# Optimization experiments

Hardware: AMD Instinct MI355X
Metric: run time of the kernel (lower is better)

## Reference

```python
import jax, jax.numpy as jnp
import numpy as np
import math

MAX_REL_POS = 32  # max_relative_position

def _sincos_table(d_model, max_len):
    pos = np.arange(max_len)[:, None].astype(np.float32)
    div = np.exp(np.arange(0, d_model, 2).astype(np.float32) * (-math.log(10000.0) / d_model))
    pe = np.zeros((max_len, d_model), dtype=np.float32)
    pe[:, 0::2] = np.sin(pos * div)
    pe[:, 1::2] = np.cos(pos * div)
    return jnp.asarray(pe)

def setup_inputs() -> dict:
    rng = jax.random.key(0)
    k1, k2, k3 = jax.random.split(rng, 3)
    B, H, S, D = 4, 16, 1024, 64
    pe = _sincos_table(D, 2 * MAX_REL_POS + 1)  # fixed (non-trainable) buffer
    return {
        "query": jax.random.normal(k1, (B, H, S, D), jnp.float32),
        "key": jax.random.normal(k2, (B, H, S, D), jnp.float32),
        "value": jax.random.normal(k3, (B, H, S, D), jnp.float32),
        "pe_k": pe,
        "pe_v": pe,
    }

def reference(query, key, value, pe_k, pe_v):
    B, H, S, D = query.shape
    # relative distance indices: clip(k - q, -P, P) + P  -> [S, S]
    dist = jnp.clip(jnp.arange(S)[None, :] - jnp.arange(S)[:, None],
                    -MAX_REL_POS, MAX_REL_POS) + MAX_REL_POS
    R_k = pe_k[dist]  # [S, S, D]
    R_v = pe_v[dist]  # [S, S, D]
    scores = jnp.einsum('bhqd,bhkd->bhqk', query, key)
    scores = scores + jnp.einsum('bhqd,qkd->bhqk', query, R_k)
    scores = scores / math.sqrt(D)
    # one_direction=True -> causal mask
    causal = jnp.tril(jnp.ones((S, S), dtype=bool))
    scores = jnp.where(causal[None, None], scores, jnp.float32(-1e9))
    p_attn = jax.nn.softmax(scores, axis=-1)
    output = jnp.einsum('bhqk,bhkd->bhqd', p_attn, value)
    output = output + jnp.einsum('bhqv,qvd->bhqd', p_attn, R_v)
    return output, p_attn
```

## Files before the change

### kernel.cpp

```cpp
#include <hip/hip_runtime.h>
#include <math.h>

typedef __attribute__((ext_vector_type(8))) short bfrag;
typedef __attribute__((ext_vector_type(4))) float ffrag;

namespace {
constexpr int Sc = 1024, Dc = 64;
constexpr int P2 = 72;
constexpr int PQ = 64;
constexpr int PW = 33;
constexpr float S2 = 0.125f * 1.44269504088896f;
}

__device__ __forceinline__ unsigned short f2bf(float f) {
    unsigned u = __builtin_bit_cast(unsigned, f);
    u += 0x7fffu + ((u >> 16) & 1u);
    return (unsigned short)(u >> 16);
}
__device__ __forceinline__ bfrag pack8(float4 a, float4 b) {
    bfrag r;
    r[0] = (short)f2bf(a.x); r[1] = (short)f2bf(a.y);
    r[2] = (short)f2bf(a.z); r[3] = (short)f2bf(a.w);
    r[4] = (short)f2bf(b.x); r[5] = (short)f2bf(b.y);
    r[6] = (short)f2bf(b.z); r[7] = (short)f2bf(b.w);
    return r;
}
#define MFMA(a, b, c) __builtin_amdgcn_mfma_f32_16x16x32_bf16((a), (b), (c), 0, 0, 0)

__global__ __launch_bounds__(256, 2)
void relattn(const float* __restrict__ Qg, const float* __restrict__ Kg,
             const float* __restrict__ Vg, const float* __restrict__ pek,
             const float* __restrict__ pev, float* __restrict__ outg,
             float* __restrict__ pbuf)
{
    __shared__ __align__(16) char smem[72448];
    unsigned short* Ks0 = (unsigned short*)smem;
    unsigned short* Ks1 = (unsigned short*)(smem + 9216);
    unsigned short* Vt0 = (unsigned short*)(smem + 18432);
    unsigned short* Vt1 = (unsigned short*)(smem + 27648);
    unsigned short* Pt0 = (unsigned short*)(smem + 36864);
    unsigned short* Pt1 = (unsigned short*)(smem + 46080);
    float* Ts = (float*)(smem + 55296);
    unsigned short* Qs = (unsigned short*)(smem + 63744);
    float* Ws = (float*)(smem + 63744);
    float* W0 = (float*)(smem + 72192);
    float* Ot = (float*)smem;

    const int tid  = threadIdx.x;
    const int bh   = blockIdx.y;
    const int wv   = tid >> 6;
    const int lane = tid & 63;
    const int n    = lane & 15;
    const int quad = lane >> 4;

    const float* Qbh = Qg + (size_t)bh * Sc * Dc;
    const float* Kbh = Kg + (size_t)bh * Sc * Dc;
    const float* Vbh = Vg + (size_t)bh * Sc * Dc;
    float* pbh = pbuf + (size_t)bh * Sc * Sc;
    float* obh = outg + (size_t)bh * Sc * Dc;

    const int sr  = tid >> 2;
    const int sc4 = (tid & 3) * 16;
    const int kp  = tid & 31;
    const int vd0 = (tid >> 5) * 8;

    const int rr = tid >> 4;
    const int c4 = tid & 15;

    for (int half = 0; half < 2; ++half) {
        const int qt = half ? (15 - (int)blockIdx.x) : (int)blockIdx.x;
        const int qrow = wv * 16 + quad * 4;

        __syncthreads();

        {
            const float* src = Qbh + (size_t)(qt * 64 + sr) * Dc + sc4;
            float4 a = *(const float4*)(src);
            float4 b = *(const float4*)(src + 4);
            float4 c = *(const float4*)(src + 8);
            float4 d = *(const float4*)(src + 12);
            *(bfrag*)&Qs[sr * PQ + sc4]     = pack8(a, b);
            *(bfrag*)&Qs[sr * PQ + sc4 + 8] = pack8(c, d);
        }
        for (int i = tid; i < 135; i += 256) {
            bfrag z = {};
            *(bfrag*)&Ks0[33 * P2 + i * 8] = z;
        }
        if (tid < 132) {
            int r = tid >> 2, c0 = (tid & 3) * 16;
            const float* src = pek + (size_t)r * Dc + c0;
            float4 a = *(const float4*)(src);
            float4 b = *(const float4*)(src + 4);
            float4 c = *(const float4*)(src + 8);
            float4 d = *(const float4*)(src + 12);
            *(bfrag*)&Ks0[r * P2 + c0]     = pack8(a, b);
            *(bfrag*)&Ks0[r * P2 + c0 + 8] = pack8(c, d);
        }
        __syncthreads();

        bfrag qa0 = *(bfrag*)&Qs[(wv * 16 + n) * PQ + quad * 8];
        bfrag qa1 = *(bfrag*)&Qs[(wv * 16 + n) * PQ + 32 + quad * 8];

        #pragma unroll
        for (int sub = 0; sub < 3; ++sub) {
            bfrag b0 = *(bfrag*)&Ks0[(sub * 16 + n) * P2 + quad * 8];
            bfrag b1 = *(bfrag*)&Ks0[(sub * 16 + n) * P2 + 32 + quad * 8];
            ffrag c = {};
            c = MFMA(qa0, b0, c);
            c = MFMA(qa1, b1, c);
            int j = sub * 16 + n;
            if (j <= 32) {
                #pragma unroll
                for (int reg = 0; reg < 4; ++reg)
                    Ts[(qrow + reg) * PW + j] = c[reg];
            }
        }
        __syncthreads();

        float ts2[4];
        #pragma unroll
        for (int reg = 0; reg < 4; ++reg) ts2[reg] = Ts[(qrow + reg) * PW] * S2;

        for (int idx = tid; idx < 64 * PW; idx += 256) Ws[idx] = 0.f;

        {
            const int zb = (qt + 1) * 64;
            if (zb < Sc) {
                const int z4 = (Sc - zb) >> 2;
                const float4 z = make_float4(0.f, 0.f, 0.f, 0.f);
                for (int r = 0; r < 64; ++r) {
                    float4* rp = (float4*)(pbh + (size_t)(qt * 64 + r) * Sc + zb);
                    for (int cz = tid; cz < z4; cz += 256) rp[cz] = z;
                }
            }
        }

        float lsum[4] = {0.f, 0.f, 0.f, 0.f};
        {
            const float* kfp = Kbh + (size_t)n * Dc + quad * 8;
            for (int kt = 0; kt <= qt; ++kt) {
                const bool bnd = (kt >= qt - 1);
                const float* kpt = kfp + (size_t)(kt * 64) * Dc;
                float4 r0[4], r1[4], r2[4], r3[4];
                #pragma unroll
                for (int s = 0; s < 4; ++s) {
                    const float* ps = kpt + (size_t)(s * 16) * Dc;
                    r0[s] = *(const float4*)(ps);
                    r1[s] = *(const float4*)(ps + 4);
                    r2[s] = *(const float4*)(ps + 32);
                    r3[s] = *(const float4*)(ps + 36);
                }
                #pragma unroll
                for (int s = 0; s < 4; ++s) {
                    bfrag b0 = pack8(r0[s], r1[s]);
                    bfrag b1 = pack8(r2[s], r3[s]);
                    ffrag c = {};
                    c = MFMA(qa0, b0, c);
                    c = MFMA(qa1, b1, c);
                    const int k = kt * 64 + s * 16 + n;
                    if (!bnd) {
                        #pragma unroll
                        for (int reg = 0; reg < 4; ++reg)
                            lsum[reg] += exp2f(fmaf(c[reg], S2, ts2[reg]));
                    } else {
                        #pragma unroll
                        for (int reg = 0; reg < 4; ++reg) {
                            int jrel = k - (qt * 64 + qrow + reg) + 32;
                            if (jrel <= 32) {
                                int jcl = jrel < 0 ? 0 : jrel;
                                lsum[reg] += exp2f(fmaf(c[reg] + Ts[(qrow + reg) * PW + jcl], S2, 0.f));
                            }
                        }
                    }
                }
            }
        }
        float rinv[4];
        #pragma unroll
        for (int reg = 0; reg < 4; ++reg) {
            float l = lsum[reg];
            l += __shfl_xor(l, 1);
            l += __shfl_xor(l, 2);
            l += __shfl_xor(l, 4);
            l += __shfl_xor(l, 8);
            rinv[reg] = 1.f / l;
        }

        {
            const float* ksrc = Kbh + (size_t)sr * Dc + sc4;
            float4 a = *(const float4*)(ksrc);
            float4 b = *(const float4*)(ksrc + 4);
            float4 c = *(const float4*)(ksrc + 8);
            float4 d = *(const float4*)(ksrc + 12);
            *(bfrag*)&Ks0[sr * P2 + sc4]     = pack8(a, b);
            *(bfrag*)&Ks0[sr * P2 + sc4 + 8] = pack8(c, d);
        }
        float4 pka, pkb, pkc, pkd;
        if (qt >= 1) {
            const float* ksrc = Kbh + (size_t)(64 + sr) * Dc + sc4;
            pka = *(const float4*)(ksrc);
            pkb = *(const float4*)(ksrc + 4);
            pkc = *(const float4*)(ksrc + 8);
            pkd = *(const float4*)(ksrc + 12);
        }
        float4 pva, pvb, pvc, pvd;
        {
            const float* vsrc = Vbh + (size_t)(2 * kp) * Dc + vd0;
            pva = *(const float4*)(vsrc);
            pvb = *(const float4*)(vsrc + 4);
            pvc = *(const float4*)(vsrc + Dc);
            pvd = *(const float4*)(vsrc + Dc + 4);
        }
        __syncthreads();

        ffrag oacc[4];
        #pragma unroll
        for (int i = 0; i < 4; ++i) { ffrag z = {}; oacc[i] = z; }

        for (int kt = 0; kt <= qt; ++kt) {
            const bool bnd = (kt >= qt - 1);
            unsigned short* Kc  = (kt & 1) ? Ks1 : Ks0;
            unsigned short* Kn  = (kt & 1) ? Ks0 : Ks1;
            unsigned short* Vc  = (kt & 1) ? Vt1 : Vt0;
            unsigned short* Vp  = (kt & 1) ? Vt0 : Vt1;
            unsigned short* Ptc = (kt & 1) ? Pt1 : Pt0;
            unsigned short* Ptp = (kt & 1) ? Pt0 : Pt1;

            #pragma unroll
            for (int sub = 0; sub < 4; ++sub) {
                bfrag b0 = *(bfrag*)&Kc[(sub * 16 + n) * P2 + quad * 8];
                bfrag b1 = *(bfrag*)&Kc[(sub * 16 + n) * P2 + 32 + quad * 8];
                ffrag c = {};
                c = MFMA(qa0, b0, c);
                c = MFMA(qa1, b1, c);
                const int k = kt * 64 + sub * 16 + n;
                if (!bnd) {
                    #pragma unroll
                    for (int reg = 0; reg < 4; ++reg) {
                        float p = exp2f(fmaf(c[reg], S2, ts2[reg])) * rinv[reg];
                        Ptc[(qrow + reg) * P2 + sub * 16 + n] = (unsigned short)f2bf(p);
                    }
                } else {
                    #pragma unroll
                    for (int reg = 0; reg < 4; ++reg) {
                        int jrel = k - (qt * 64 + qrow + reg) + 32;
                        float p = 0.f;
                        if (jrel <= 32) {
                            int jcl = jrel < 0 ? 0 : jrel;
                            p = exp2f((c[reg] + Ts[(qrow + reg) * PW + jcl]) * S2) * rinv[reg];
                        }
                        Ptc[(qrow + reg) * P2 + sub * 16 + n] = (unsigned short)f2bf(p);
                        if ((unsigned)(jrel - 1) < 32u) Ws[(qrow + reg) * PW + jrel - 1] = p;
                    }
                }
            }
            if (kt < qt) {
                *(bfrag*)&Kn[sr * P2 + sc4]     = pack8(pka, pkb);
                *(bfrag*)&Kn[sr * P2 + sc4 + 8] = pack8(pkc, pkd);
            }
            {
                float r0[8] = {pva.x, pva.y, pva.z, pva.w, pvb.x, pvb.y, pvb.z, pvb.w};
                float r1[8] = {pvc.x, pvc.y, pvc.z, pvc.w, pvd.x, pvd.y, pvd.z, pvd.w};
                #pragma unroll
                for (int i = 0; i < 8; ++i) {
                    unsigned pk2 = (unsigned)f2bf(r0[i]) | ((unsigned)f2bf(r1[i]) << 16);
                    *(unsigned*)&Vc[(vd0 + i) * P2 + 2 * kp] = pk2;
                }
            }
            if (kt + 2 <= qt) {
                const float* ksrc = Kbh + (size_t)((kt + 2) * 64 + sr) * Dc + sc4;
                pka = *(const float4*)(ksrc);
                pkb = *(const float4*)(ksrc + 4);
                pkc = *(const float4*)(ksrc + 8);
                pkd = *(const float4*)(ksrc + 12);
            }
            if (kt + 1 <= qt) {
                const float* vsrc = Vbh + (size_t)((kt + 1) * 64 + 2 * kp) * Dc + vd0;
                pva = *(const float4*)(vsrc);
                pvb = *(const float4*)(vsrc + 4);
                pvc = *(const float4*)(vsrc + Dc);
                pvd = *(const float4*)(vsrc + Dc + 4);
            }
            if (kt >= 1) {
                bfrag pb0 = *(bfrag*)&Ptp[(wv * 16 + n) * P2 + quad * 8];
                bfrag pb1 = *(bfrag*)&Ptp[(wv * 16 + n) * P2 + 32 + quad * 8];
                #pragma unroll
                for (int ds = 0; ds < 4; ++ds) {
                    bfrag va0 = *(bfrag*)&Vp[(ds * 16 + n) * P2 + quad * 8];
                    bfrag va1 = *(bfrag*)&Vp[(ds * 16 + n) * P2 + 32 + quad * 8];
                    oacc[ds] = MFMA(va0, pb0, oacc[ds]);
                    oacc[ds] = MFMA(va1, pb1, oacc[ds]);
                }
                float* base = pbh + ((size_t)(qt * 64 + rr) * Sc + (kt - 1) * 64 + c4 * 4);
                #pragma unroll
                for (int step = 0; step < 4; ++step) {
                    const int r = step * 16 + rr;
                    uint2 two = *(const uint2*)&Ptp[r * P2 + c4 * 4];
                    float4 v;
                    v.x = __builtin_bit_cast(float, (two.x & 0xffffu) << 16);
                    v.y = __builtin_bit_cast(float, two.x & 0xffff0000u);
                    v.z = __builtin_bit_cast(float, (two.y & 0xffffu) << 16);
                    v.w = __builtin_bit_cast(float, two.y & 0xffff0000u);
                    *(float4*)(base + (size_t)(step * 16) * Sc) = v;
                }
            }
            __syncthreads();
        }
        {
            unsigned short* Ptp = (qt & 1) ? Pt1 : Pt0;
            unsigned short* Vp  = (qt & 1) ? Vt1 : Vt0;
            bfrag pb0 = *(bfrag*)&Ptp[(wv * 16 + n) * P2 + quad * 8];
            bfrag pb1 = *(bfrag*)&Ptp[(wv * 16 + n) * P2 + 32 + quad * 8];
            #pragma unroll
            for (int ds = 0; ds < 4; ++ds) {
                bfrag va0 = *(bfrag*)&Vp[(ds * 16 + n) * P2 + quad * 8];
                bfrag va1 = *(bfrag*)&Vp[(ds * 16 + n) * P2 + 32 + quad * 8];
                oacc[ds] = MFMA(va0, pb0, oacc[ds]);
                oacc[ds] = MFMA(va1, pb1, oacc[ds]);
            }
            float* base = pbh + ((size_t)(qt * 64 + rr) * Sc + qt * 64 + c4 * 4);
            #pragma unroll
            for (int step = 0; step < 4; ++step) {
                const int r = step * 16 + rr;
                uint2 two = *(const uint2*)&Ptp[r * P2 + c4 * 4];
                float4 v;
                v.x = __builtin_bit_cast(float, (two.x & 0xffffu) << 16);
                v.y = __builtin_bit_cast(float, two.x & 0xffff0000u);
                v.z = __builtin_bit_cast(float, (two.y & 0xffffu) << 16);
                v.w = __builtin_bit_cast(float, two.y & 0xffff0000u);
                *(float4*)(base + (size_t)(step * 16) * Sc) = v;
            }
        }
        __syncthreads();

        if (tid < 64) {
            float s = 0.f;
            #pragma unroll
            for (int j = 0; j < 32; ++j) s += Ws[tid * PW + j];
            W0[tid] = 1.f - s;
        }
        {
            int q = tid >> 2, j0 = (tid & 3) * 8;
            #pragma unroll
            for (int i = 0; i < 8; i += 2) {
                unsigned pk2 = (unsigned)f2bf(Ws[q * PW + j0 + i]) |
                               ((unsigned)f2bf(Ws[q * PW + j0 + i + 1]) << 16);
                *(unsigned*)&Pt0[q * P2 + j0 + i] = pk2;
            }
        }
        {
            int jj = tid >> 3, d0 = (tid & 7) * 8;
            const float* src = pev + (size_t)(jj + 1) * Dc + d0;
            float4 a = *(const float4*)(src);
            float4 b = *(const float4*)(src + 4);
            float vr[8] = {a.x, a.y, a.z, a.w, b.x, b.y, b.z, b.w};
            #pragma unroll
            for (int i = 0; i < 8; ++i)
                Vt0[(d0 + i) * P2 + jj] = (unsigned short)f2bf(vr[i]);
        }
        __syncthreads();
        {
            bfrag pb = *(bfrag*)&Pt0[(wv * 16 + n) * P2 + quad * 8];
            #pragma unroll
            for (int ds = 0; ds < 4; ++ds) {
                bfrag va = *(bfrag*)&Vt0[(ds * 16 + n) * P2 + quad * 8];
                oacc[ds] = MFMA(va, pb, oacc[ds]);
            }
        }
        float w0q = W0[wv * 16 + n];
        #pragma unroll
        for (int ds = 0; ds < 4; ++ds) {
            float4 ov;
            ov.x = oacc[ds][0] + w0q * pev[ds * 16 + quad * 4 + 0];
            ov.y = oacc[ds][1] + w0q * pev[ds * 16 + quad * 4 + 1];
            ov.z = oacc[ds][2] + w0q * pev[ds * 16 + quad * 4 + 2];
            ov.w = oacc[ds][3] + w0q * pev[ds * 16 + quad * 4 + 3];
            *(float4*)&Ot[(wv * 16 + n) * 68 + ds * 16 + quad * 4] = ov;
        }
        __syncthreads();
        {
            int r = tid >> 2, c0 = (tid & 3) * 16;
            float* dst = obh + (size_t)(qt * 64 + r) * Dc + c0;
            *(float4*)(dst)      = *(float4*)&Ot[r * 68 + c0];
            *(float4*)(dst + 4)  = *(float4*)&Ot[r * 68 + c0 + 4];
            *(float4*)(dst + 8)  = *(float4*)&Ot[r * 68 + c0 + 8];
            *(float4*)(dst + 12) = *(float4*)&Ot[r * 68 + c0 + 12];
        }
    }
}

extern "C" void kernel_launch(void* const* d_in, const int* in_sizes, int n_in,
                              void* d_out, int out_size, void* d_ws, size_t ws_size,
                              hipStream_t stream)
{
    const float* Q   = (const float*)d_in[0];
    const float* K   = (const float*)d_in[1];
    const float* V   = (const float*)d_in[2];
    const float* pek = (const float*)d_in[3];
    const float* pev = (const float*)d_in[4];
    float* out  = (float*)d_out;
    float* pbuf = out + (size_t)64 * Sc * Dc;

    dim3 grid(8, 64);
    relattn<<<grid, 256, 0, stream>>>(Q, K, V, pek, pev, out, pbuf);
}
```

Before: 411.4 us.

## Stage K tiles through shared memory in the row-sum pass

The first pass, which computes the softmax row sums, used to have each wave load its own K fragments straight from global memory and convert them per wave. It now loads each K tile cooperatively into shared memory as bf16, in groups of three tiles. The groups are double-buffered across the Ks, Vt and Pt buffers, with register prefetch of the next group. This removes redundant global loads across the four waves, at the cost of extra shared-memory traffic, a barrier per group, and more registers held for prefetch.

```diff
diff --git a/kernel.cpp b/kernel.cpp
--- a/kernel.cpp
+++ b/kernel.cpp
@@ -73,6 +73,17 @@
 
         __syncthreads();
 
+        float4 pka[3], pkb[3], pkc[3], pkd[3];
+        #pragma unroll
+        for (int t = 0; t < 3; ++t) {
+            if (t <= qt) {
+                const float* ksrc = Kbh + (size_t)(t * 64 + sr) * Dc + sc4;
+                pka[t] = *(const float4*)(ksrc);
+                pkb[t] = *(const float4*)(ksrc + 4);
+                pkc[t] = *(const float4*)(ksrc + 8);
+                pkd[t] = *(const float4*)(ksrc + 12);
+            }
+        }
         {
             const float* src = Qbh + (size_t)(qt * 64 + sr) * Dc + sc4;
             float4 a = *(const float4*)(src);
@@ -84,7 +95,7 @@
         }
         for (int i = tid; i < 135; i += 256) {
             bfrag z = {};
-            *(bfrag*)&Ks0[33 * P2 + i * 8] = z;
+            *(bfrag*)&Pt1[33 * P2 + i * 8] = z;
         }
         if (tid < 132) {
             int r = tid >> 2, c0 = (tid & 3) * 16;
@@ -93,8 +104,8 @@
             float4 b = *(const float4*)(src + 4);
             float4 c = *(const float4*)(src + 8);
             float4 d = *(const float4*)(src + 12);
-            *(bfrag*)&Ks0[r * P2 + c0]     = pack8(a, b);
-            *(bfrag*)&Ks0[r * P2 + c0 + 8] = pack8(c, d);
+            *(bfrag*)&Pt1[r * P2 + c0]     = pack8(a, b);
+            *(bfrag*)&Pt1[r * P2 + c0 + 8] = pack8(c, d);
         }
         __syncthreads();
 
@@ -103,8 +114,8 @@
 
         #pragma unroll
         for (int sub = 0; sub < 3; ++sub) {
-            bfrag b0 = *(bfrag*)&Ks0[(sub * 16 + n) * P2 + quad * 8];
-            bfrag b1 = *(bfrag*)&Ks0[(sub * 16 + n) * P2 + 32 + quad * 8];
+            bfrag b0 = *(bfrag*)&Pt1[(sub * 16 + n) * P2 + quad * 8];
+            bfrag b1 = *(bfrag*)&Pt1[(sub * 16 + n) * P2 + 32 + quad * 8];
             ffrag c = {};
             c = MFMA(qa0, b0, c);
             c = MFMA(qa1, b1, c);
@@ -115,6 +126,24 @@
                     Ts[(qrow + reg) * PW + j] = c[reg];
             }
         }
+        #pragma unroll
+        for (int t = 0; t < 3; ++t) {
+            if (t <= qt) {
+                unsigned short* Bn = t == 0 ? Ks0 : (t == 1 ? Ks1 : Vt0);
+                *(bfrag*)&Bn[sr * P2 + sc4]     = pack8(pka[t], pkb[t]);
+                *(bfrag*)&Bn[sr * P2 + sc4 + 8] = pack8(pkc[t], pkd[t]);
+            }
+        }
+        #pragma unroll
+        for (int t = 0; t < 3; ++t) {
+            if (3 + t <= qt) {
+                const float* ksrc = Kbh + (size_t)((3 + t) * 64 + sr) * Dc + sc4;
+                pka[t] = *(const float4*)(ksrc);
+                pkb[t] = *(const float4*)(ksrc + 4);
+                pkc[t] = *(const float4*)(ksrc + 8);
+                pkd[t] = *(const float4*)(ksrc + 12);
+            }
+        }
         __syncthreads();
 
         float ts2[4];
@@ -136,44 +165,64 @@
         }
 
         float lsum[4] = {0.f, 0.f, 0.f, 0.f};
-        {
-            const float* kfp = Kbh + (size_t)n * Dc + quad * 8;
-            for (int kt = 0; kt <= qt; ++kt) {
-                const bool bnd = (kt >= qt - 1);
-                const float* kpt = kfp + (size_t)(kt * 64) * Dc;
-                float4 r0[4], r1[4], r2[4], r3[4];
-                #pragma unroll
-                for (int s = 0; s < 4; ++s) {
-                    const float* ps = kpt + (size_t)(s * 16) * Dc;
-                    r0[s] = *(const float4*)(ps);
-                    r1[s] = *(const float4*)(ps + 4);
-                    r2[s] = *(const float4*)(ps + 32);
-                    r3[s] = *(const float4*)(ps + 36);
-                }
-                #pragma unroll
-                for (int s = 0; s < 4; ++s) {
-                    bfrag b0 = pack8(r0[s], r1[s]);
-                    bfrag b1 = pack8(r2[s], r3[s]);
-                    ffrag c = {};
-                    c = MFMA(qa0, b0, c);
-                    c = MFMA(qa1, b1, c);
-                    const int k = kt * 64 + s * 16 + n;
-                    if (!bnd) {
-                        #pragma unroll
-                        for (int reg = 0; reg < 4; ++reg)
-                            lsum[reg] += exp2f(fmaf(c[reg], S2, ts2[reg]));
-                    } else {
-                        #pragma unroll
-                        for (int reg = 0; reg < 4; ++reg) {
-                            int jrel = k - (qt * 64 + qrow + reg) + 32;
-                            if (jrel <= 32) {
-                                int jcl = jrel < 0 ? 0 : jrel;
-                                lsum[reg] += exp2f(fmaf(c[reg] + Ts[(qrow + reg) * PW + jcl], S2, 0.f));
+        for (int kt = 0; kt <= qt; kt += 3) {
+            const int ph = (kt / 3) & 1;
+            unsigned short* Bc0 = ph ? Vt1 : Ks0;
+            unsigned short* Bc1 = ph ? Pt0 : Ks1;
+            unsigned short* Bc2 = ph ? Pt1 : Vt0;
+            unsigned short* Bn0 = ph ? Ks0 : Vt1;
+            unsigned short* Bn1 = ph ? Ks1 : Pt0;
+            unsigned short* Bn2 = ph ? Vt0 : Pt1;
+
+            #pragma unroll
+            for (int t = 0; t < 3; ++t) {
+                if (kt + t <= qt) {
+                    unsigned short* Bc = t == 0 ? Bc0 : (t == 1 ? Bc1 : Bc2);
+                    const bool bnd = (kt + t >= qt - 1);
+                    #pragma unroll
+                    for (int sub = 0; sub < 4; ++sub) {
+                        bfrag b0 = *(bfrag*)&Bc[(sub * 16 + n) * P2 + quad * 8];
+                        bfrag b1 = *(bfrag*)&Bc[(sub * 16 + n) * P2 + 32 + quad * 8];
+                        ffrag c = {};
+                        c = MFMA(qa0, b0, c);
+                        c = MFMA(qa1, b1, c);
+                        const int k = (kt + t) * 64 + sub * 16 + n;
+                        if (!bnd) {
+                            #pragma unroll
+                            for (int reg = 0; reg < 4; ++reg)
+                                lsum[reg] += exp2f(fmaf(c[reg], S2, ts2[reg]));
+                        } else {
+                            #pragma unroll
+                            for (int reg = 0; reg < 4; ++reg) {
+                                int jrel = k - (qt * 64 + qrow + reg) + 32;
+                                if (jrel <= 32) {
+                                    int jcl = jrel < 0 ? 0 : jrel;
+                                    lsum[reg] += exp2f(fmaf(c[reg] + Ts[(qrow + reg) * PW + jcl], S2, 0.f));
+                                }
                             }
                         }
                     }
                 }
             }
+            #pragma unroll
+            for (int t = 0; t < 3; ++t) {
+                if (kt + 3 + t <= qt) {
+                    unsigned short* Bn = t == 0 ? Bn0 : (t == 1 ? Bn1 : Bn2);
+                    *(bfrag*)&Bn[sr * P2 + sc4]     = pack8(pka[t], pkb[t]);
+                    *(bfrag*)&Bn[sr * P2 + sc4 + 8] = pack8(pkc[t], pkd[t]);
+                }
+            }
+            #pragma unroll
+            for (int t = 0; t < 3; ++t) {
+                if (kt + 6 + t <= qt) {
+                    const float* ksrc = Kbh + (size_t)((kt + 6 + t) * 64 + sr) * Dc + sc4;
+                    pka[t] = *(const float4*)(ksrc);
+                    pkb[t] = *(const float4*)(ksrc + 4);
+                    pkc[t] = *(const float4*)(ksrc + 8);
+                    pkd[t] = *(const float4*)(ksrc + 12);
+                }
+            }
+            __syncthreads();
         }
         float rinv[4];
         #pragma unroll
@@ -195,13 +244,12 @@
             *(bfrag*)&Ks0[sr * P2 + sc4]     = pack8(a, b);
             *(bfrag*)&Ks0[sr * P2 + sc4 + 8] = pack8(c, d);
         }
-        float4 pka, pkb, pkc, pkd;
         if (qt >= 1) {
             const float* ksrc = Kbh + (size_t)(64 + sr) * Dc + sc4;
-            pka = *(const float4*)(ksrc);
-            pkb = *(const float4*)(ksrc + 4);
-            pkc = *(const float4*)(ksrc + 8);
-            pkd = *(const float4*)(ksrc + 12);
+            pka[0] = *(const float4*)(ksrc);
+            pkb[0] = *(const float4*)(ksrc + 4);
+            pkc[0] = *(const float4*)(ksrc + 8);
+            pkd[0] = *(const float4*)(ksrc + 12);
         }
         float4 pva, pvb, pvc, pvd;
         {
@@ -255,8 +303,8 @@
                 }
             }
             if (kt < qt) {
-                *(bfrag*)&Kn[sr * P2 + sc4]     = pack8(pka, pkb);
-                *(bfrag*)&Kn[sr * P2 + sc4 + 8] = pack8(pkc, pkd);
+                *(bfrag*)&Kn[sr * P2 + sc4]     = pack8(pka[0], pkb[0]);
+                *(bfrag*)&Kn[sr * P2 + sc4 + 8] = pack8(pkc[0], pkd[0]);
             }
             {
                 float r0[8] = {pva.x, pva.y, pva.z, pva.w, pvb.x, pvb.y, pvb.z, pvb.w};
@@ -269,10 +317,10 @@
             }
             if (kt + 2 <= qt) {
                 const float* ksrc = Kbh + (size_t)((kt + 2) * 64 + sr) * Dc + sc4;
-                pka = *(const float4*)(ksrc);
-                pkb = *(const float4*)(ksrc + 4);
-                pkc = *(const float4*)(ksrc + 8);
-                pkd = *(const float4*)(ksrc + 12);
+                pka[0] = *(const float4*)(ksrc);
+                pkb[0] = *(const float4*)(ksrc + 4);
+                pkc[0] = *(const float4*)(ksrc + 8);
+                pkd[0] = *(const float4*)(ksrc + 12);
             }
             if (kt + 1 <= qt) {
                 const float* vsrc = Vbh + (size_t)((kt + 1) * 64 + 2 * kp) * Dc + vd0;
```

New measurement: 387.0 us. 5.9% less time.
